# Optimization experiments

Measured on AMD Instinct MI355X. Metric: run time of the kernel, lower is better.

The kernel has to match this reference:

```python
import jax, jax.numpy as jnp
import numpy as np

B, N, F = 2, 2048, 256
H = 8
O = F // H  # nhid = 32
L = 3       # stacked GraphAttentionLayers
ALPHA = 0.2
NEG = jnp.float32(-1e15)


def setup_inputs() -> dict:
    key = jax.random.key(0)
    ks = jax.random.split(key, 6)
    x = jax.random.normal(ks[0], (B, N, F), dtype=jnp.float32)
    adj = jax.random.randint(ks[1], (B, N, N), 0, 2, dtype=jnp.int32)
    # per-layer multi-head params: W [L,H,F,O], a [L,H,2O]
    W_heads = jax.random.normal(ks[2], (L, H, F, O), dtype=jnp.float32) * 0.1
    a_heads = jax.random.normal(ks[3], (L, H, 2 * O), dtype=jnp.float32) * 0.1
    # per-layer out_att params (single head, F->F)
    W_out = jax.random.normal(ks[4], (L, F, F), dtype=jnp.float32) * 0.05
    a_out = jax.random.normal(ks[5], (L, 2 * F), dtype=jnp.float32) * 0.05
    return {"x": x, "adj": adj, "W_heads": W_heads, "a_heads": a_heads,
            "W_out": W_out, "a_out": a_out}


def _gat_heads(h, mask, W, a1, a2):
    """h: [B,N,F], mask: [B,N,N] bool, W: [H,F,O], a1/a2: [H,O] -> [B,H,N,O]."""
    Wh = jnp.einsum('bnf,hfo->bhno', h, W)
    s1 = jnp.einsum('bhno,ho->bhn', Wh, a1)   # a[:O] projection
    s2 = jnp.einsum('bhno,ho->bhn', Wh, a2)   # a[O:] projection
    e = s1[:, :, :, None] + s2[:, :, None, :]  # additive score [B,H,N,N]
    e = jnp.where(e > 0, e, ALPHA * e)         # LeakyReLU(alpha)
    e = jnp.where(mask[:, None, :, :], e, NEG)
    att = jax.nn.softmax(e, axis=-1)           # dropout is identity in eval
    hp = jnp.einsum('bhnm,bhmo->bhno', att, Wh)
    return jax.nn.elu(hp)                      # activate_function inside head


def reference(x, adj, W_heads, a_heads, W_out, a_out):
    mask = adj > 0
    h = x
    for l in range(L):
        a1 = a_heads[l, :, :O]
        a2 = a_heads[l, :, O:]
        hh = _gat_heads(h, mask, W_heads[l], a1, a2)      # [B,H,N,O]
        h = jnp.transpose(hh, (0, 2, 1, 3)).reshape(B, N, F)  # concat heads
        ao1 = a_out[l, :F][None]
        ao2 = a_out[l, F:][None]
        ho = _gat_heads(h, mask, W_out[l][None], ao1, ao2)[:, 0]  # [B,N,F]
        h = jax.nn.elu(ho)  # extra F.elu in GraphAttentionLayer (elu twice)
    return h
```

## Files before the change

kernel.cpp:

```cpp
#include <hip/hip_runtime.h>
#include <math.h>

#if __has_builtin(__builtin_amdgcn_exp2f)
#define EXP2(x) __builtin_amdgcn_exp2f(x)
#else
#define EXP2(x) exp2f(x)
#endif

#define ALPHA_LRELU 0.2f
#define LOG2E 1.4426950408889634f
#define ESHIFT 6.0f
#define BIGM 1024.0f

constexpr int Bc = 2, Nn = 2048, Ff = 256, Hh = 8, Oo = 32;

typedef _Float16 f16;
typedef f16 f16x8 __attribute__((ext_vector_type(8)));
typedef f16 f16x4 __attribute__((ext_vector_type(4)));
typedef float f32x4 __attribute__((ext_vector_type(4)));
typedef unsigned long long u64;
typedef unsigned u32;

__global__ __launch_bounds__(256) void prep_kernel(
    const int* __restrict__ adj, const float* __restrict__ x,
    const float* __restrict__ W_heads, const float* __restrict__ W_out,
    u32* __restrict__ maskT, f16* __restrict__ Af, f16* __restrict__ WTF,
    float* __restrict__ sbuf) {
    const int B = blockIdx.x;
    const int t = threadIdx.x;
    int g = B * 256 + t;
    if (g < 221184) sbuf[g] = 0.f;

    if (B < 768) {
        for (int idx = g; idx < Bc * Nn * Nn; idx += 768 * 256) {
            u64 bl = __ballot(adj[idx] != 0);
            int lane = t & 63;
            int i = (idx >> 11) & 2047;
            int b = idx >> 22;
            int c32 = ((idx & 2047) & ~63) >> 5;
            if (lane == 0)
                maskT[((size_t)b * 64 + c32) * 2048 + i] = (u32)bl;
            else if (lane == 1)
                maskT[((size_t)b * 64 + c32 + 1) * 2048 + i] = (u32)(bl >> 32);
        }
    } else if (B < 896) {
        int w = t >> 6, lane = t & 63;
        int am = lane & 15, aq = lane >> 4;
#pragma unroll
        for (int it = 0; it < 4; ++it) {
            int slot = (B - 768) * 4 + w + it * 512;
            int mt = slot >> 3, c = slot & 7;
            const float* ap = x + ((size_t)mt * 16 + am) * Ff + c * 32 + aq * 8;
            f32x4 v0 = *(const f32x4*)ap;
            f32x4 v1 = *(const f32x4*)(ap + 4);
            f16x8 o;
#pragma unroll
            for (int i = 0; i < 4; ++i) { o[i] = (f16)v0[i]; o[4 + i] = (f16)v1[i]; }
            *(f16x8*)&Af[(size_t)slot * 512 + lane * 8] = o;
        }
    } else {
#pragma unroll
        for (int it = 0; it < 3; ++it) {
            int unit = (B - 896) * 3 + it;
            int y = unit >> 6, bx = unit & 63;
            int ll = y >> 1, st = y & 1;
            int col = bx * 4 + (t >> 6);
            int k0 = (t & 63) * 4;
            const float* src;
            int stride;
            if (st == 0) {
                src = W_heads + (((size_t)ll * Hh + (col >> 5)) * Ff) * Oo + (col & 31);
                stride = Oo;
            } else {
                src = W_out + (size_t)ll * Ff * Ff + col;
                stride = Ff;
            }
            f16x4 v;
#pragma unroll
            for (int i = 0; i < 4; ++i) v[i] = (f16)src[(size_t)(k0 + i) * stride];
            int cg = col >> 4, am = col & 15;
            int c = k0 >> 5, aq = (k0 >> 3) & 3, i0 = k0 & 7;
            *(f16x4*)&WTF[(((size_t)y * 16 + cg) * 8 + c) * 512 +
                          (aq * 16 + am) * 8 + i0] = v;
        }
    }
}

__global__ __launch_bounds__(256) void gemm_wave(
    const f16* __restrict__ Af, const f16* __restrict__ WTF,
    const float* __restrict__ pa, f16* __restrict__ WhFrag,
    float* __restrict__ s1, float* __restrict__ s2,
    int G, int Ofull, int oshift) {
    int t = threadIdx.x;
    int w = t >> 6, lane = t & 63;
    int am = lane & 15, aq = lane >> 4;
    int mt = blockIdx.x * 4 + w;
    int colb = blockIdx.y * 32;

    const f16* ap = Af + (size_t)(mt * 8) * 512 + lane * 8;
    const f16* bp0 = WTF + (size_t)((colb >> 4) * 8) * 512 + lane * 8;
    const f16* bp1 = bp0 + 8 * 512;

    f16x8 av[8], bv0[8], bv1[8];
#pragma unroll
    for (int c = 0; c < 8; ++c) {
        av[c] = *(const f16x8*)(ap + c * 512);
        bv0[c] = *(const f16x8*)(bp0 + c * 512);
        bv1[c] = *(const f16x8*)(bp1 + c * 512);
    }
    f32x4 acc0 = {0.f, 0.f, 0.f, 0.f}, acc1 = acc0;
#pragma unroll
    for (int c = 0; c < 8; ++c) {
        acc0 = __builtin_amdgcn_mfma_f32_16x16x32_f16(av[c], bv0[c], acc0, 0, 0, 0);
        acc1 = __builtin_amdgcn_mfma_f32_16x16x32_f16(av[c], bv1[c], acc1, 0, 0, 0);
    }

    int m0 = mt * 16;
    int b = m0 >> 11;
    int nn0 = (m0 & 2047) + aq * 4;
    int cO = (m0 & 2047) >> 5;
    int aq_p = ((mt & 1) << 1) | (aq >> 1);
    int i0p = (aq & 1) << 2;
    int g = colb >> oshift;
    size_t bg = (size_t)b * G + g;
    int cg = (colb & (Ofull - 1)) >> 4;

    f16x4 c40, c41;
#pragma unroll
    for (int e = 0; e < 4; ++e) { c40[e] = (f16)acc0[e]; c41[e] = (f16)acc1[e]; }
    *(f16x4*)&WhFrag[(((bg * (Ofull >> 4) + cg) * 64 + cO) * 512) +
                     (aq_p * 16 + am) * 8 + i0p] = c40;
    *(f16x4*)&WhFrag[(((bg * (Ofull >> 4) + cg + 1) * 64 + cO) * 512) +
                     (aq_p * 16 + am) * 8 + i0p] = c41;

    int o0 = (colb & (Ofull - 1)) + am;
    const float* a1p = pa + 2 * (size_t)g * Ofull;
    float a10 = a1p[o0], a11 = a1p[o0 + 16];
    float a20 = a1p[Ofull + o0], a21 = a1p[Ofull + o0 + 16];
#pragma unroll
    for (int e = 0; e < 4; ++e) {
        float p1 = acc0[e] * a10 + acc1[e] * a11;
        float p2 = acc0[e] * a20 + acc1[e] * a21;
#pragma unroll
        for (int s = 1; s < 16; s <<= 1) {
            p1 += __shfl_xor(p1, s);
            p2 += __shfl_xor(p2, s);
        }
        if (am == 0) {
            size_t sidx = bg * Nn + nn0 + e;
            atomicAdd(&s1[sidx], p1);
            atomicAdd(&s2[sidx], p2);
        }
    }
}

template <int CGW, int NW, bool OUT, bool FINAL>
__global__ __launch_bounds__(NW * 64) void attn_kernel(
    const f16* __restrict__ WhFrag, const float* __restrict__ s1,
    const float* __restrict__ s2, const u32* __restrict__ maskT,
    float* __restrict__ dst, f16* __restrict__ AfOut) {
    constexpr float C0 = -ESHIFT * LOG2E - BIGM;
    constexpr float C08 = (1.0f - ALPHA_LRELU) * C0;
    constexpr int NCG = OUT ? 16 : 2;
    constexpr int COLS = (NW / 4) * CGW * 16;
    constexpr int TSTR = COLS + 8;
    __shared__ float Ls[NW][2][64];
    __shared__ float As[NW][64][2 * CGW * 4];
    __shared__ f16 T[2][16 * TSTR];

    int t = threadIdx.x;
    int w = t >> 6, lane = t & 63;
    int am = lane & 15, aq = lane >> 4;
    int ch = w >> 2;
    int js = w & 3;
    int i0 = blockIdx.x * 32;
    int bz = blockIdx.z;
    int b = OUT ? bz : (bz >> 3);
    int cg0 = OUT ? blockIdx.y * ((NW / 4) * CGW) + ch * CGW : 0;
    int dstcol = OUT ? cg0 * 16 : (bz & 7) * Oo;

    const f16* bp[CGW];
#pragma unroll
    for (int i = 0; i < CGW; ++i)
        bp[i] = WhFrag + ((size_t)bz * NCG + cg0 + i) * 64 * 512 + lane * 8;
    const float* s2p = s2 + (size_t)bz * Nn + aq * 8;
    float s1c0 = fmaf(s1[(size_t)bz * Nn + i0 + am], LOG2E, C0);
    float s1c1 = fmaf(s1[(size_t)bz * Nn + i0 + 16 + am], LOG2E, C0);
    const u32* mtp0 = maskT + (size_t)b * 64 * 2048 + i0 + am;
    const u32* mtp1 = mtp0 + 16;

    f32x4 acc[2][CGW] = {};
    float lacc0 = 0.f, lacc1 = 0.f;

    int cbeg = js * 16, cend = cbeg + 16;

    f16x8 xb[CGW], yb[CGW];
    f32x4 xv0, xv1, yv0, yv1;
    u32 xm0, xm1, ym0, ym1;
    auto ld = [&](int c, f16x8 (&bb)[CGW], f32x4& v0, f32x4& v1,
                  u32& m0, u32& m1) {
#pragma unroll
        for (int i = 0; i < CGW; ++i) bb[i] = *(const f16x8*)(bp[i] + c * 512);
        v0 = *(const f32x4*)(s2p + c * 32);
        v1 = *(const f32x4*)(s2p + c * 32 + 4);
        m0 = mtp0[c * 2048];
        m1 = mtp1[c * 2048];
    };
    auto comp = [&](f16x8 (&bb)[CGW], f32x4 v0, f32x4 v1, u32 m0, u32 m1) {
        u32 bits0 = (m0 >> (aq * 8)) & 0xffu;
        u32 bits1 = (m1 >> (aq * 8)) & 0xffu;
        f16x8 af0, af1;
#pragma unroll
        for (int k = 0; k < 8; ++k) {
            float svl = (k < 4 ? v0[k] : v1[k - 4]) * LOG2E;
            float u0 = s1c0 + svl;
            float u1 = s1c1 + svl;
            float lr0 = fmaxf(u0, fmaf(ALPHA_LRELU, u0, C08));
            float lr1 = fmaxf(u1, fmaf(ALPHA_LRELU, u1, C08));
            float bf0 = (float)((bits0 >> k) & 1u);
            float bf1 = (float)((bits1 >> k) & 1u);
            float p0 = EXP2(fmaf(bf0, BIGM, lr0));
            float p1 = EXP2(fmaf(bf1, BIGM, lr1));
            lacc0 += p0;
            lacc1 += p1;
            af0[k] = (f16)p0;
            af1[k] = (f16)p1;
        }
#pragma unroll
        for (int i = 0; i < CGW; ++i) {
            acc[0][i] = __builtin_amdgcn_mfma_f32_16x16x32_f16(af0, bb[i], acc[0][i], 0, 0, 0);
            acc[1][i] = __builtin_amdgcn_mfma_f32_16x16x32_f16(af1, bb[i], acc[1][i], 0, 0, 0);
        }
    };

    ld(cbeg, xb, xv0, xv1, xm0, xm1);
    ld(cbeg + 1, yb, yv0, yv1, ym0, ym1);
    for (int c = cbeg; c < cend; c += 2) {
        comp(xb, xv0, xv1, xm0, xm1);
        ld(c + 2 < cend ? c + 2 : cbeg, xb, xv0, xv1, xm0, xm1);
        comp(yb, yv0, yv1, ym0, ym1);
        ld(c + 3 < cend ? c + 3 : cbeg, yb, yv0, yv1, ym0, ym1);
    }

    lacc0 += __shfl_xor(lacc0, 16);
    lacc0 += __shfl_xor(lacc0, 32);
    lacc1 += __shfl_xor(lacc1, 16);
    lacc1 += __shfl_xor(lacc1, 32);

    Ls[w][0][lane] = lacc0;
    Ls[w][1][lane] = lacc1;
#pragma unroll
    for (int tt = 0; tt < 2; ++tt)
#pragma unroll
        for (int i = 0; i < CGW; ++i)
#pragma unroll
            for (int e = 0; e < 4; ++e)
                As[w][lane][tt * CGW * 4 + i * 4 + e] = acc[tt][i][e];
    __syncthreads();

    if ((w & 3) < 2) {
        int tt = w & 3;
        float lt = Ls[ch * 4 + 0][tt][lane] + Ls[ch * 4 + 1][tt][lane] +
                   Ls[ch * 4 + 2][tt][lane] + Ls[ch * 4 + 3][tt][lane];
        float rli[4];
#pragma unroll
        for (int e = 0; e < 4; ++e) rli[e] = 1.0f / __shfl(lt, aq * 4 + e);
        f16* Tw = T[tt];
#pragma unroll
        for (int i = 0; i < CGW; ++i) {
            f32x4 a;
#pragma unroll
            for (int e = 0; e < 4; ++e)
                a[e] = As[ch * 4 + 0][lane][tt * CGW * 4 + i * 4 + e] +
                       As[ch * 4 + 1][lane][tt * CGW * 4 + i * 4 + e] +
                       As[ch * 4 + 2][lane][tt * CGW * 4 + i * 4 + e] +
                       As[ch * 4 + 3][lane][tt * CGW * 4 + i * 4 + e];
#pragma unroll
            for (int e = 0; e < 4; ++e) {
                int r = aq * 4 + e;
                float v = a[e] * rli[e];
                v = v > 0.f ? v : __expf(v) - 1.f;
                if (OUT) v = v > 0.f ? v : __expf(v) - 1.f;
                if (FINAL) {
                    dst[((size_t)b * Nn + i0 + tt * 16 + r) * Ff + dstcol +
                        i * 16 + am] = v;
                } else {
                    Tw[r * TSTR + ch * CGW * 16 + i * 16 + am] = (f16)v;
                }
            }
        }
        if (!FINAL) {
            int mt = (b * Nn + i0 + tt * 16) >> 4;
#pragma unroll
            for (int s = 0; s < CGW / 2; ++s) {
                f16x8 o = *(const f16x8*)&Tw[am * TSTR + ch * CGW * 16 +
                                             s * 32 + aq * 8];
                int c = (dstcol >> 5) + s;
                *(f16x8*)&AfOut[(size_t)(mt * 8 + c) * 512 + lane * 8] = o;
            }
        }
    }
}

extern "C" void kernel_launch(void* const* d_in, const int* in_sizes, int n_in,
                              void* d_out, int out_size, void* d_ws, size_t ws_size,
                              hipStream_t stream) {
    const float* x = (const float*)d_in[0];
    const int* adj = (const int*)d_in[1];
    const float* W_heads = (const float*)d_in[2];
    const float* a_heads = (const float*)d_in[3];
    const float* W_out = (const float*)d_in[4];
    const float* a_out = (const float*)d_in[5];
    float* out = (float*)d_out;

    float* ws = (float*)d_ws;
    const size_t M = (size_t)Bc * Nn * Ff;
    f16* Af_a = (f16*)ws;
    f16* Af_b = (f16*)(ws + M / 2);
    f16* WhFrag = (f16*)(ws + M);
    u32* maskT = (u32*)(ws + 3 * M / 2);
    f16* WTF = (f16*)(ws + 3 * M / 2 + M / 4);
    float* sbuf = ws + 3 * M / 2 + M / 4 + 196608;
    const size_t SH = (size_t)Bc * Hh * Nn;
    const size_t SO = (size_t)Bc * Nn;
    const size_t SL = 2 * SH + 2 * SO;

    prep_kernel<<<1024, 256, 0, stream>>>(adj, x, W_heads, W_out,
                                          maskT, Af_a, WTF, sbuf);

    for (int l = 0; l < 3; ++l) {
        float* s1h = sbuf + l * SL;
        float* s2h = s1h + SH;
        float* s1o = s2h + SH;
        float* s2o = s1o + SO;

        gemm_wave<<<dim3((Bc * Nn) / 64, Ff / 32), 256, 0, stream>>>(
            Af_a, WTF + (size_t)(2 * l) * Ff * Ff,
            a_heads + (size_t)l * Hh * 2 * Oo, WhFrag, s1h, s2h, Hh, Oo, 5);
        attn_kernel<2, 4, false, false><<<dim3(Nn / 32, 1, Bc * Hh), 256, 0, stream>>>(
            WhFrag, s1h, s2h, maskT, nullptr, Af_b);

        gemm_wave<<<dim3((Bc * Nn) / 64, Ff / 32), 256, 0, stream>>>(
            Af_b, WTF + (size_t)(2 * l + 1) * Ff * Ff,
            a_out + (size_t)l * 2 * Ff, WhFrag, s1o, s2o, 1, Ff, 8);
        if (l == 2) {
            attn_kernel<4, 8, true, true><<<dim3(Nn / 32, Ff / 128, Bc), 512, 0, stream>>>(
                WhFrag, s1o, s2o, maskT, out, nullptr);
        } else {
            attn_kernel<4, 8, true, false><<<dim3(Nn / 32, Ff / 128, Bc), 512, 0, stream>>>(
                WhFrag, s1o, s2o, maskT, nullptr, Af_a);
        }
    }
}
```

Before: 259.0 us.

## Compute softmax row sums via MFMA with ones and mask exp by bitwise AND

```diff
diff --git a/kernel.cpp b/kernel.cpp
--- a/kernel.cpp
+++ b/kernel.cpp
@@ -10,7 +10,6 @@
 #define ALPHA_LRELU 0.2f
 #define LOG2E 1.4426950408889634f
 #define ESHIFT 6.0f
-#define BIGM 1024.0f
 
 constexpr int Bc = 2, Nn = 2048, Ff = 256, Hh = 8, Oo = 32;
 
@@ -148,8 +147,13 @@
         }
         if (am == 0) {
             size_t sidx = bg * Nn + nn0 + e;
-            atomicAdd(&s1[sidx], p1);
-            atomicAdd(&s2[sidx], p2);
+            if (G == 1) {
+                atomicAdd(&s1[sidx], p1);
+                atomicAdd(&s2[sidx], p2 * LOG2E);
+            } else {
+                s1[sidx] = p1;
+                s2[sidx] = p2 * LOG2E;
+            }
         }
     }
 }
@@ -159,7 +163,7 @@
     const f16* __restrict__ WhFrag, const float* __restrict__ s1,
     const float* __restrict__ s2, const u32* __restrict__ maskT,
     float* __restrict__ dst, f16* __restrict__ AfOut) {
-    constexpr float C0 = -ESHIFT * LOG2E - BIGM;
+    constexpr float C0 = -ESHIFT * LOG2E;
     constexpr float C08 = (1.0f - ALPHA_LRELU) * C0;
     constexpr int NCG = OUT ? 16 : 2;
     constexpr int COLS = (NW / 4) * CGW * 16;
@@ -190,7 +194,10 @@
     const u32* mtp1 = mtp0 + 16;
 
     f32x4 acc[2][CGW] = {};
-    float lacc0 = 0.f, lacc1 = 0.f;
+    f32x4 accL0 = {0.f, 0.f, 0.f, 0.f}, accL1 = accL0;
+    f16x8 ones;
+#pragma unroll
+    for (int i = 0; i < 8; ++i) ones[i] = (f16)1.0f;
 
     int cbeg = js * 16, cend = cbeg + 16;
 
@@ -212,20 +219,20 @@
         f16x8 af0, af1;
 #pragma unroll
         for (int k = 0; k < 8; ++k) {
-            float svl = (k < 4 ? v0[k] : v1[k - 4]) * LOG2E;
-            float u0 = s1c0 + svl;
-            float u1 = s1c1 + svl;
+            float sv = (k < 4 ? v0[k] : v1[k - 4]);
+            float u0 = s1c0 + sv;
+            float u1 = s1c1 + sv;
             float lr0 = fmaxf(u0, fmaf(ALPHA_LRELU, u0, C08));
             float lr1 = fmaxf(u1, fmaf(ALPHA_LRELU, u1, C08));
-            float bf0 = (float)((bits0 >> k) & 1u);
-            float bf1 = (float)((bits1 >> k) & 1u);
-            float p0 = EXP2(fmaf(bf0, BIGM, lr0));
-            float p1 = EXP2(fmaf(bf1, BIGM, lr1));
-            lacc0 += p0;
-            lacc1 += p1;
+            u32 z0 = 0u - ((bits0 >> k) & 1u);
+            u32 z1 = 0u - ((bits1 >> k) & 1u);
+            float p0 = __uint_as_float(__float_as_uint(EXP2(lr0)) & z0);
+            float p1 = __uint_as_float(__float_as_uint(EXP2(lr1)) & z1);
             af0[k] = (f16)p0;
             af1[k] = (f16)p1;
         }
+        accL0 = __builtin_amdgcn_mfma_f32_16x16x32_f16(af0, ones, accL0, 0, 0, 0);
+        accL1 = __builtin_amdgcn_mfma_f32_16x16x32_f16(af1, ones, accL1, 0, 0, 0);
 #pragma unroll
         for (int i = 0; i < CGW; ++i) {
             acc[0][i] = __builtin_amdgcn_mfma_f32_16x16x32_f16(af0, bb[i], acc[0][i], 0, 0, 0);
@@ -242,13 +249,13 @@
         ld(c + 3 < cend ? c + 3 : cbeg, yb, yv0, yv1, ym0, ym1);
     }
 
-    lacc0 += __shfl_xor(lacc0, 16);
-    lacc0 += __shfl_xor(lacc0, 32);
-    lacc1 += __shfl_xor(lacc1, 16);
-    lacc1 += __shfl_xor(lacc1, 32);
-
-    Ls[w][0][lane] = lacc0;
-    Ls[w][1][lane] = lacc1;
+    if (am == 0) {
+#pragma unroll
+        for (int e = 0; e < 4; ++e) {
+            Ls[w][0][aq * 4 + e] = accL0[e];
+            Ls[w][1][aq * 4 + e] = accL1[e];
+        }
+    }
 #pragma unroll
     for (int tt = 0; tt < 2; ++tt)
 #pragma unroll
```

New measurement: 280.0 us. 8.1% more time.
